# Performance work log

Measured on AMD Instinct MI355X. Metric: run time of the kernel, lower is better.

Reference implementation:

```python
import jax, jax.numpy as jnp
import numpy as np

HEADS = 16
DIM_HEAD = 64
SEG = 512            # total_segment_len (num_longterm_mem_tokens = 0)
THETA = 10000.0
NEG_INF = -1e30


def _rotate_half(t):
    # interleaved pair rotation, as in rotary-embedding-torch
    t2 = t.reshape(*t.shape[:-1], t.shape[-1] // 2, 2)
    return jnp.stack((-t2[..., 1], t2[..., 0]), axis=-1).reshape(t.shape)


def setup_inputs() -> dict:
    key = jax.random.key(0)
    ks = jax.random.split(key, 4)
    b, n, d = 2, 4096, 1024
    dim_inner = HEADS * DIM_HEAD
    seq = jax.random.normal(ks[0], (b, n, d), dtype=jnp.float32)
    g_norm = jnp.ones((d,), dtype=jnp.float32)
    W_qkv = jax.random.normal(ks[1], (d, 3 * dim_inner), dtype=jnp.float32) * (d ** -0.5)
    W_out = jax.random.normal(ks[2], (dim_inner, d), dtype=jnp.float32) * (dim_inner ** -0.5)
    pm = jax.random.normal(ks[3], (2, HEADS, 16, DIM_HEAD), dtype=jnp.float32) * 0.02
    return {"seq": seq, "g_norm": g_norm, "W_qkv": W_qkv, "W_out": W_out, "pm": pm}


def reference(seq, g_norm, W_qkv, W_out, pm):
    b, n_tot, dim = seq.shape
    p = pm.shape[2]
    dh = DIM_HEAD

    # RMSNorm (elementwise affine, eps = dtype eps as in torch default)
    eps = jnp.asarray(jnp.finfo(seq.dtype).eps, seq.dtype)
    x = seq * jax.lax.rsqrt(jnp.mean(seq * seq, axis=-1, keepdims=True) + eps) * g_norm

    qkv = x @ W_qkv                                   # [b, n, 3*h*dh]
    q, k, v = jnp.split(qkv, 3, axis=-1)

    def split_heads(t):
        return t.reshape(b, n_tot, HEADS, dh).transpose(0, 2, 1, 3)  # b h n d

    q, k, v = map(split_heads, (q, k, v))

    # rotary over global positions (applied before segmenting)
    pos = jnp.arange(n_tot, dtype=seq.dtype)
    inv_freq = 1.0 / (THETA ** (jnp.arange(0, dh, 2, dtype=seq.dtype) / dh))
    ang = jnp.repeat(pos[:, None] * inv_freq, 2, axis=-1)            # [n, dh]
    cos, sin = jnp.cos(ang), jnp.sin(ang)
    q = q * cos + _rotate_half(q) * sin
    k = k * cos + _rotate_half(k) * sin

    # fold segments into batch: b h (w n) d -> (b w) h n d
    w = n_tot // SEG
    def seg_fold(t):
        return t.reshape(b, HEADS, w, SEG, dh).transpose(0, 2, 1, 3, 4).reshape(b * w, HEADS, SEG, dh)
    q, k, v = map(seg_fold, (q, k, v))

    # prepend persistent memory kv
    pmk = jnp.broadcast_to(pm[0], (b * w, HEADS, p, dh))
    pmv = jnp.broadcast_to(pm[1], (b * w, HEADS, p, dh))
    k = jnp.concatenate((pmk, k), axis=-2)            # [(bw), h, p+n, d]
    v = jnp.concatenate((pmv, v), axis=-2)

    scores = jnp.einsum('bhid,bhjd->bhij', q, k) * (dh ** -0.5)
    i = jnp.arange(SEG)[:, None]
    j = jnp.arange(SEG + p)[None, :]
    mask = (j < p) | ((j - p) <= i)                   # persistent mem always visible, causal in-segment
    scores = jnp.where(mask, scores, NEG_INF)
    attn = jax.nn.softmax(scores, axis=-1)
    out = jnp.einsum('bhij,bhjd->bhid', attn, v)      # [(bw), h, n, d]

    out = out.transpose(0, 2, 1, 3).reshape(b * w, SEG, HEADS * dh)
    out = out @ W_out
    return out.reshape(b, n_tot, dim)
```

## Files before the change

kernel.cpp:

```cpp
#include <hip/hip_runtime.h>
#include <hip/hip_bf16.h>

typedef __attribute__((ext_vector_type(8))) short short8v;
typedef __attribute__((ext_vector_type(4))) float f32x4;

#define B_ 2
#define NTOK 4096
#define DMODEL 1024
#define HEADS_ 16
#define DH 64
#define SEG_ 512
#define PMEM 16
#define ROWS 8192
#define QKVC 3072

__global__ __launch_bounds__(256) void rmsnorm_bf16(const float* __restrict__ seq,
                                                    const float* __restrict__ g,
                                                    __hip_bfloat16* __restrict__ x) {
    int row = blockIdx.x;
    const float4* in = (const float4*)(seq + (size_t)row * DMODEL);
    int tid = threadIdx.x;
    float4 v = in[tid];
    float ss = v.x*v.x + v.y*v.y + v.z*v.z + v.w*v.w;
    #pragma unroll
    for (int off = 32; off >= 1; off >>= 1) ss += __shfl_xor(ss, off, 64);
    __shared__ float red[4];
    if ((tid & 63) == 0) red[tid >> 6] = ss;
    __syncthreads();
    float tot = red[0] + red[1] + red[2] + red[3];
    float scale = rsqrtf(tot * (1.0f/(float)DMODEL) + 1.1920929e-7f);
    float4 gv = ((const float4*)g)[tid];
    union { ushort4 u; __hip_bfloat16 h[4]; } pk;
    pk.h[0] = __float2bfloat16(v.x*scale*gv.x);
    pk.h[1] = __float2bfloat16(v.y*scale*gv.y);
    pk.h[2] = __float2bfloat16(v.z*scale*gv.z);
    pk.h[3] = __float2bfloat16(v.w*scale*gv.w);
    ((ushort4*)(x + (size_t)row * DMODEL))[tid] = pk.u;
}

__global__ __launch_bounds__(256) void setup_kernel(float* __restrict__ tab,
                                                    const float* __restrict__ pm,
                                                    __hip_bfloat16* __restrict__ pmb,
                                                    const float* __restrict__ wqkv,
                                                    __hip_bfloat16* __restrict__ wqkvt,
                                                    const float* __restrict__ wout,
                                                    __hip_bfloat16* __restrict__ woutt) {
    __shared__ float t[32][33];
    int b = blockIdx.x;
    if (b < 640) {
        int idx = b*256 + threadIdx.x;
        if (idx < NTOK*32) {
            int n = idx >> 5, p = idx & 31;
            float inv = powf(10000.f, -(float)p * (1.f/32.f));
            float a = (float)n * inv;
            float sn, cs;
            sincosf(a, &sn, &cs);
            float* tp = tab + (size_t)n*64;
            tp[2*p]     = cs;
            tp[2*p + 1] = sn;
        } else {
            int j = idx - NTOK*32;
            pmb[j] = __float2bfloat16(pm[j]);
        }
        return;
    }
    b -= 640;
    const float* W; __hip_bfloat16* Wt; int N, n0, k0;
    if (b < 3072) { W = wqkv; Wt = wqkvt; N = QKVC;   n0 = (b % 96)*32; k0 = (b / 96)*32; }
    else { b -= 3072; W = wout; Wt = woutt; N = DMODEL; n0 = (b % 32)*32; k0 = (b / 32)*32; }
    int c = threadIdx.x & 31, r = threadIdx.x >> 5;
    #pragma unroll
    for (int rr = 0; rr < 32; rr += 8)
        t[rr + r][c] = W[(size_t)(k0 + rr + r)*N + n0 + c];
    __syncthreads();
    #pragma unroll
    for (int rr = 0; rr < 32; rr += 8)
        Wt[(size_t)(n0 + rr + r)*DMODEL + k0 + c] = __float2bfloat16(t[c][rr + r]);
}

__device__ __forceinline__ void gldl(const __hip_bfloat16* g, char* l) {
    __builtin_amdgcn_global_load_lds((const __attribute__((address_space(1))) void*)g,
                                     (__attribute__((address_space(3))) void*)l, 16, 0, 0);
}
__device__ __forceinline__ void storeC(float* p, float v) { *p = v; }
__device__ __forceinline__ void storeC(__hip_bfloat16* p, float v) { *p = __float2bfloat16(v); }

template<typename OutT, bool ROPE>
__global__ __launch_bounds__(256, 2) void gemm_t(const __hip_bfloat16* __restrict__ A,
                                                 const __hip_bfloat16* __restrict__ Bt,
                                                 OutT* __restrict__ C,
                                                 const float* __restrict__ tab,
                                                 int M, int N, int K) {
    __shared__ __align__(16) char smem[32768];
    const int tid = threadIdx.x;
    const int wid = tid >> 6, lane = tid & 63;
    const int q8 = gridDim.x >> 3;
    const int swz = (blockIdx.x & 7) * q8 + (blockIdx.x >> 3);
    const int nbx = N >> 7;
    const int bm = (swz / nbx) * 128, bn = (swz % nbx) * 128;
    const int wm = (wid >> 1) * 64, wn = (wid & 1) * 64;
    const int fr = lane & 15, g = lane >> 4;

    const int srow = tid >> 3;
    const int scol = ((tid & 7) ^ (srow & 7)) * 8;
    const __hip_bfloat16* Asrc = A  + (size_t)(bm + srow)*K + scol;
    const __hip_bfloat16* Bsrc = Bt + (size_t)(bn + srow)*K + scol;

    f32x4 acc[4][4];
    #pragma unroll
    for (int i = 0; i < 4; ++i)
        #pragma unroll
        for (int j = 0; j < 4; ++j)
            acc[i][j] = (f32x4){0.f, 0.f, 0.f, 0.f};

    for (int k0 = 0; k0 < K; k0 += 64) {
        #pragma unroll
        for (int i = 0; i < 4; ++i)
            gldl(Asrc + (size_t)i*32*K + k0, smem + i*4096 + tid*16);
        #pragma unroll
        for (int i = 0; i < 4; ++i)
            gldl(Bsrc + (size_t)i*32*K + k0, smem + 16384 + i*4096 + tid*16);
        __syncthreads();

        short8v a[4][2], b[4][2];
        #pragma unroll
        for (int mt = 0; mt < 4; ++mt) {
            int row = wm + mt*16 + fr;
            #pragma unroll
            for (int ks = 0; ks < 2; ++ks)
                a[mt][ks] = *(const short8v*)(smem + row*128 + ((ks*64 + g*16) ^ ((fr&7)<<4)));
        }
        #pragma unroll
        for (int nt = 0; nt < 4; ++nt) {
            int row = wn + nt*16 + fr;
            #pragma unroll
            for (int ks = 0; ks < 2; ++ks)
                b[nt][ks] = *(const short8v*)(smem + 16384 + row*128 + ((ks*64 + g*16) ^ ((fr&7)<<4)));
        }
        #pragma unroll
        for (int mt = 0; mt < 4; ++mt)
            #pragma unroll
            for (int nt = 0; nt < 4; ++nt)
                #pragma unroll
                for (int ks = 0; ks < 2; ++ks)
                    acc[mt][nt] = __builtin_amdgcn_mfma_f32_16x16x32_bf16(a[mt][ks], b[nt][ks], acc[mt][nt], 0, 0, 0);
        __syncthreads();
    }

    const int rsub = (lane >> 4) << 2;
    if (ROPE && bn < 2048) {
        #pragma unroll
        for (int mt = 0; mt < 4; ++mt) {
            int rbase = bm + wm + mt*16 + rsub;
            #pragma unroll
            for (int nt = 0; nt < 4; ++nt) {
                int col = bn + wn + nt*16 + fr;
                int d = col & 63;
                int dc = d & ~1;
                #pragma unroll
                for (int r = 0; r < 4; ++r) {
                    float v = acc[mt][nt][r];
                    float pv = __shfl_xor(v, 1, 64);
                    int n = (rbase + r) & (NTOK - 1);
                    const float* tb = tab + (size_t)n*64;
                    float cs = tb[dc], sn = tb[dc+1];
                    float o = v*cs + ((d & 1) ? pv*sn : -pv*sn);
                    storeC(&C[(size_t)(rbase + r)*N + col], (float)o);
                }
            }
        }
    } else {
        #pragma unroll
        for (int mt = 0; mt < 4; ++mt) {
            int rbase = bm + wm + mt*16 + rsub;
            #pragma unroll
            for (int nt = 0; nt < 4; ++nt) {
                int col = bn + wn + nt*16 + fr;
                #pragma unroll
                for (int r = 0; r < 4; ++r)
                    storeC(&C[(size_t)(rbase + r)*N + col], acc[mt][nt][r]);
            }
        }
    }
}

__device__ __forceinline__ void stage_load(const __hip_bfloat16* __restrict__ qkv,
                                           const __hip_bfloat16* __restrict__ pmb,
                                           int h, int srow, int tt, int skey, int sdg,
                                           uint4 kv[2]) {
    int kg = tt*64 + skey;
    if (kg < PMEM) {
        kv[0] = *(const uint4*)(pmb + ((size_t)h*PMEM + kg)*DH + sdg);
        kv[1] = *(const uint4*)(pmb + ((size_t)(HEADS_ + h)*PMEM + kg)*DH + sdg);
    } else {
        int r = min(kg - PMEM, SEG_ - 1);
        const __hip_bfloat16* bp = qkv + (size_t)(srow + r)*QKVC + h*DH + sdg;
        kv[0] = *(const uint4*)(bp + 1024);
        kv[1] = *(const uint4*)(bp + 2048);
    }
}

__device__ __forceinline__ void stage_write(char* Kb, char* Vb,
                                            int skey, int sdg, const uint4 kv[2]) {
    *(uint4*)(Kb + ((skey*128 + sdg*2) ^ ((skey&7)<<4))) = kv[0];
    union { uint4 u; ushort s[8]; } vv; vv.u = kv[1];
    #pragma unroll
    for (int j = 0; j < 8; ++j) {
        int d = sdg + j;
        *(ushort*)(Vb + ((d*128 + skey*2) ^ ((d&7)<<4))) = vv.s[j];
    }
}

__global__ __launch_bounds__(512, 2) void attn_mfma(const __hip_bfloat16* __restrict__ qkv,
                                                    const __hip_bfloat16* __restrict__ pmb,
                                                    __hip_bfloat16* __restrict__ ao) {
    __shared__ __hip_bfloat16 KB[2][4096];
    __shared__ __hip_bfloat16 VB[2][4096];
    __shared__ __hip_bfloat16 PB[8][1024];

    const int bid = blockIdx.x;
    const int xcd = bid & 7, ii = bid >> 3;
    const int s  = 2*xcd + (ii >> 5);
    const int h  = ii & 15;
    const int rb = (ii >> 4) & 1;
    const int srow = (s >> 3)*NTOK + (s & 7)*SEG_;
    const int tid = threadIdx.x;
    const int w = tid >> 6, lane = tid & 63;
    const int g = lane >> 4, fr = lane & 15;
    const int rsub = g * 4;
    char* Pw = (char*)&PB[w][0];

    const int grp0 = 2*w + rb;
    const int grp1 = 30 - 2*w + rb;
    const int tmax = 7 + rb;

    short8v aq[2][2];
    #pragma unroll
    for (int mt = 0; mt < 2; ++mt) {
        int grp = mt ? grp1 : grp0;
        const __hip_bfloat16* qp = qkv + (size_t)(srow + grp*16 + fr)*QKVC + h*DH;
        #pragma unroll
        for (int ks = 0; ks < 2; ++ks)
            aq[mt][ks] = *(const short8v*)(qp + ks*32 + g*8);
    }

    f32x4 accO[2][4];
    float l_[2][4];
    #pragma unroll
    for (int mt = 0; mt < 2; ++mt) {
        #pragma unroll
        for (int dt = 0; dt < 4; ++dt) accO[mt][dt] = (f32x4){0.f,0.f,0.f,0.f};
        #pragma unroll
        for (int r = 0; r < 4; ++r) l_[mt][r] = 0.f;
    }

    const int skey = tid >> 3, sdg = (tid & 7) * 8;

    {
        uint4 kv[2];
        stage_load(qkv, pmb, h, srow, 0, skey, sdg, kv);
        stage_write((char*)&KB[0][0], (char*)&VB[0][0], skey, sdg, kv);
    }
    __syncthreads();

    for (int t = 0; t <= tmax; ++t) {
        const int bf = t & 1;
        uint4 kvn[2];
        if (t < tmax) stage_load(qkv, pmb, h, srow, t + 1, skey, sdg, kvn);

        char* Kb = (char*)&KB[bf][0];
        char* Vb = (char*)&VB[bf][0];

        short8v bk[4][2];
        #pragma unroll
        for (int nt = 0; nt < 4; ++nt)
            #pragma unroll
            for (int ks = 0; ks < 2; ++ks) {
                int row = nt*16 + fr;
                bk[nt][ks] = *(const short8v*)(Kb + ((row*128 + ks*64 + g*16) ^ ((row&7)<<4)));
            }

        #pragma unroll
        for (int mt = 0; mt < 2; ++mt) {
            const int qb = (mt ? grp1 : grp0) * 16;
            if (t > 0 && t*64 > qb + 31) continue;

            f32x4 sA[4];
            #pragma unroll
            for (int nt = 0; nt < 4; ++nt) sA[nt] = (f32x4){0.f,0.f,0.f,0.f};
            __builtin_amdgcn_s_setprio(1);
            #pragma unroll
            for (int ks = 0; ks < 2; ++ks)
                #pragma unroll
                for (int nt = 0; nt < 4; ++nt)
                    sA[nt] = __builtin_amdgcn_mfma_f32_16x16x32_bf16(aq[mt][ks], bk[nt][ks], sA[nt], 0, 0, 0);
            __builtin_amdgcn_s_setprio(0);

            if (!(t*64 + 63 <= qb + 16)) {
                #pragma unroll
                for (int nt = 0; nt < 4; ++nt) {
                    int kg2 = t*64 + nt*16 + fr;
                    #pragma unroll
                    for (int r = 0; r < 4; ++r) {
                        int irow = qb + rsub + r;
                        if (!((kg2 < PMEM) || (kg2 <= irow + PMEM))) sA[nt][r] = -1e30f;
                    }
                }
            }

            #pragma unroll
            for (int nt = 0; nt < 4; ++nt)
                #pragma unroll
                for (int r = 0; r < 4; ++r)
                    sA[nt][r] = __expf(fmaf(sA[nt][r], 0.125f, -8.0f));
            #pragma unroll
            for (int r = 0; r < 4; ++r)
                l_[mt][r] += sA[0][r] + sA[1][r] + sA[2][r] + sA[3][r];

            #pragma unroll
            for (int nt = 0; nt < 4; ++nt)
                #pragma unroll
                for (int r = 0; r < 4; ++r) {
                    int row_l = rsub + r;
                    *(__hip_bfloat16*)(Pw + ((row_l*128 + (nt*16 + fr)*2) ^ ((row_l&7)<<4))) =
                        __float2bfloat16(sA[nt][r]);
                }

            __builtin_amdgcn_s_setprio(1);
            #pragma unroll
            for (int ks2 = 0; ks2 < 2; ++ks2) {
                short8v ap = *(const short8v*)(Pw + ((fr*128 + ks2*64 + g*16) ^ ((fr&7)<<4)));
                #pragma unroll
                for (int dt = 0; dt < 4; ++dt) {
                    int vrow = dt*16 + fr;
                    short8v bv = *(const short8v*)(Vb + ((vrow*128 + ks2*64 + g*16) ^ ((vrow&7)<<4)));
                    accO[mt][dt] = __builtin_amdgcn_mfma_f32_16x16x32_bf16(ap, bv, accO[mt][dt], 0, 0, 0);
                }
            }
            __builtin_amdgcn_s_setprio(0);
        }

        if (t < tmax) stage_write((char*)&KB[bf^1][0], (char*)&VB[bf^1][0], skey, sdg, kvn);
        __syncthreads();
    }

    #pragma unroll
    for (int mt = 0; mt < 2; ++mt) {
        const int grp = mt ? grp1 : grp0;
        float inv[4];
        #pragma unroll
        for (int r = 0; r < 4; ++r) {
            float lt = l_[mt][r];
            #pragma unroll
            for (int off = 1; off <= 8; off <<= 1) lt += __shfl_xor(lt, off, 64);
            inv[r] = 1.0f / lt;
        }
        #pragma unroll
        for (int dt = 0; dt < 4; ++dt)
            #pragma unroll
            for (int r = 0; r < 4; ++r) {
                int row_l = rsub + r;
                *(__hip_bfloat16*)(Pw + ((row_l*128 + (dt*16 + fr)*2) ^ ((row_l&7)<<4))) =
                    __float2bfloat16(accO[mt][dt][r] * inv[r]);
            }
        #pragma unroll
        for (int c = 0; c < 2; ++c) {
            int row_l = c*8 + (lane >> 3);
            size_t grow = (size_t)(srow + grp*16 + row_l);
            uint4 v = *(const uint4*)(Pw + ((row_l*128 + (lane&7)*16) ^ ((row_l&7)<<4)));
            *(uint4*)((char*)(ao + grow*DMODEL + h*DH) + (lane&7)*16) = v;
        }
    }
}

extern "C" void kernel_launch(void* const* d_in, const int* in_sizes, int n_in,
                              void* d_out, int out_size, void* d_ws, size_t ws_size,
                              hipStream_t stream) {
    const float* seq  = (const float*)d_in[0];
    const float* g    = (const float*)d_in[1];
    const float* wqkv = (const float*)d_in[2];
    const float* wout = (const float*)d_in[3];
    const float* pm   = (const float*)d_in[4];
    float* out = (float*)d_out;

    char* ws = (char*)d_ws;
    __hip_bfloat16* qkvb  = (__hip_bfloat16*)ws;
    __hip_bfloat16* xb    = (__hip_bfloat16*)(ws + 50331648);
    __hip_bfloat16* wqkvt = (__hip_bfloat16*)(ws + 50331648 + 16777216);
    __hip_bfloat16* woutt = (__hip_bfloat16*)(ws + 50331648 + 16777216 + 6291456);
    float* tab            = (float*)(ws + 50331648 + 16777216 + 6291456 + 2097152);
    __hip_bfloat16* pmb   = (__hip_bfloat16*)(ws + 50331648 + 16777216 + 6291456 + 2097152 + 1048576);

    setup_kernel<<<4736, 256, 0, stream>>>(tab, pm, pmb, wqkv, wqkvt, wout, woutt);
    rmsnorm_bf16<<<ROWS, 256, 0, stream>>>(seq, g, xb);
    gemm_t<__hip_bfloat16, true><<<(QKVC/128)*(ROWS/128), 256, 0, stream>>>(xb, wqkvt, qkvb, tab, ROWS, QKVC, DMODEL);
    attn_mfma<<<512, 512, 0, stream>>>(qkvb, pmb, xb);
    gemm_t<float, false><<<(DMODEL/128)*(ROWS/128), 256, 0, stream>>>(xb, woutt, out, nullptr, ROWS, DMODEL, DMODEL);
}
```

Measured before the change: 147.1 us.

## Add warp-specialized producer/consumer GEMM for QKV projection with RoPE epilogue

Replaces the QKV projection GEMM with a 512-thread kernel where four producer waves stream A/B tiles from global memory through registers into double-buffered LDS, while four consumer waves run MFMA with raised priority. The intent is to overlap global loads with matrix math instead of relying on the previous global_load_lds path with per-iteration syncs. The cost is 64KB of shared memory per block, which lowers occupancy, plus more barriers per tile. The old ROPE branch is removed from gemm_t since only the output GEMM still uses it.

```diff
diff --git a/kernel.cpp b/kernel.cpp
--- a/kernel.cpp
+++ b/kernel.cpp
@@ -85,6 +85,135 @@
 __device__ __forceinline__ void storeC(float* p, float v) { *p = v; }
 __device__ __forceinline__ void storeC(__hip_bfloat16* p, float v) { *p = __float2bfloat16(v); }
 
+__global__ __launch_bounds__(512, 2) void gemm_pc(const __hip_bfloat16* __restrict__ A,
+                                                  const __hip_bfloat16* __restrict__ Bt,
+                                                  __hip_bfloat16* __restrict__ C,
+                                                  const float* __restrict__ tab) {
+    __shared__ __align__(16) char smem[65536];
+    const int tid = threadIdx.x;
+    const int wid = tid >> 6, lane = tid & 63;
+    const int q8 = gridDim.x >> 3;
+    const int swz = (blockIdx.x & 7) * q8 + (blockIdx.x >> 3);
+    const int nbx = QKVC >> 7;
+    const int bm = (swz / nbx) * 128, bn = (swz % nbx) * 128;
+    const int K = DMODEL;
+
+    if (wid >= 4) {
+        const int ptid = tid - 256;
+        const int srow = ptid >> 3;
+        const int scol = ((ptid & 7) ^ (srow & 7)) * 8;
+        const __hip_bfloat16* Asrc = A  + (size_t)(bm + srow)*K + scol;
+        const __hip_bfloat16* Bsrc = Bt + (size_t)(bn + srow)*K + scol;
+        uint4 ra[4], rb[4];
+        #pragma unroll
+        for (int i = 0; i < 4; ++i) {
+            ra[i] = *(const uint4*)(Asrc + (size_t)i*32*K);
+            rb[i] = *(const uint4*)(Bsrc + (size_t)i*32*K);
+        }
+        #pragma unroll
+        for (int i = 0; i < 4; ++i) {
+            *(uint4*)(smem + i*4096 + ptid*16) = ra[i];
+            *(uint4*)(smem + 16384 + i*4096 + ptid*16) = rb[i];
+        }
+        #pragma unroll
+        for (int i = 0; i < 4; ++i) {
+            ra[i] = *(const uint4*)(Asrc + (size_t)i*32*K + 64);
+            rb[i] = *(const uint4*)(Bsrc + (size_t)i*32*K + 64);
+        }
+        asm volatile("s_waitcnt lgkmcnt(0)" ::: "memory");
+        __builtin_amdgcn_s_barrier();
+        #pragma unroll 1
+        for (int t = 0; t < 16; ++t) {
+            if (t < 15) {
+                char* dst = smem + ((t + 1) & 1)*32768;
+                #pragma unroll
+                for (int i = 0; i < 4; ++i) {
+                    *(uint4*)(dst + i*4096 + ptid*16) = ra[i];
+                    *(uint4*)(dst + 16384 + i*4096 + ptid*16) = rb[i];
+                }
+                if (t < 14) {
+                    const int k0 = (t + 2)*64;
+                    #pragma unroll
+                    for (int i = 0; i < 4; ++i) {
+                        ra[i] = *(const uint4*)(Asrc + (size_t)i*32*K + k0);
+                        rb[i] = *(const uint4*)(Bsrc + (size_t)i*32*K + k0);
+                    }
+                }
+            }
+            asm volatile("s_waitcnt lgkmcnt(0)" ::: "memory");
+            __builtin_amdgcn_s_barrier();
+        }
+        return;
+    }
+
+    const int wm = (wid >> 1) * 64, wn = (wid & 1) * 64;
+    const int fr = lane & 15, g = lane >> 4;
+
+    f32x4 acc[4][4];
+    #pragma unroll
+    for (int i = 0; i < 4; ++i)
+        #pragma unroll
+        for (int j = 0; j < 4; ++j)
+            acc[i][j] = (f32x4){0.f, 0.f, 0.f, 0.f};
+
+    __builtin_amdgcn_s_barrier();
+    #pragma unroll 1
+    for (int t = 0; t < 16; ++t) {
+        const char* buf = smem + (t & 1)*32768;
+        short8v a[4][2], b[4][2];
+        #pragma unroll
+        for (int mt = 0; mt < 4; ++mt) {
+            int row = wm + mt*16 + fr;
+            #pragma unroll
+            for (int ks = 0; ks < 2; ++ks)
+                a[mt][ks] = *(const short8v*)(buf + row*128 + ((ks*64 + g*16) ^ ((fr&7)<<4)));
+        }
+        #pragma unroll
+        for (int nt = 0; nt < 4; ++nt) {
+            int row = wn + nt*16 + fr;
+            #pragma unroll
+            for (int ks = 0; ks < 2; ++ks)
+                b[nt][ks] = *(const short8v*)(buf + 16384 + row*128 + ((ks*64 + g*16) ^ ((fr&7)<<4)));
+        }
+        __builtin_amdgcn_s_setprio(1);
+        #pragma unroll
+        for (int mt = 0; mt < 4; ++mt)
+            #pragma unroll
+            for (int nt = 0; nt < 4; ++nt)
+                #pragma unroll
+                for (int ks = 0; ks < 2; ++ks)
+                    acc[mt][nt] = __builtin_amdgcn_mfma_f32_16x16x32_bf16(a[mt][ks], b[nt][ks], acc[mt][nt], 0, 0, 0);
+        __builtin_amdgcn_s_setprio(0);
+        __builtin_amdgcn_s_barrier();
+    }
+
+    const int rsub = (lane >> 4) << 2;
+    const bool dorope = (bn < 2048);
+    #pragma unroll
+    for (int mt = 0; mt < 4; ++mt) {
+        int rbase = bm + wm + mt*16 + rsub;
+        #pragma unroll
+        for (int nt = 0; nt < 4; ++nt) {
+            int col = bn + wn + nt*16 + fr;
+            int d = col & 63;
+            int dc = d & ~1;
+            #pragma unroll
+            for (int r = 0; r < 4; ++r) {
+                float v = acc[mt][nt][r];
+                float pv = __shfl_xor(v, 1, 64);
+                float o = v;
+                if (dorope) {
+                    int n = (rbase + r) & (NTOK - 1);
+                    const float* tb = tab + (size_t)n*64;
+                    float cs = tb[dc], sn = tb[dc+1];
+                    o = v*cs + ((d & 1) ? pv*sn : -pv*sn);
+                }
+                storeC(&C[(size_t)(rbase + r)*QKVC + col], o);
+            }
+        }
+    }
+}
+
 template<typename OutT, bool ROPE>
 __global__ __launch_bounds__(256, 2) void gemm_t(const __hip_bfloat16* __restrict__ A,
                                                  const __hip_bfloat16* __restrict__ Bt,
@@ -148,38 +277,15 @@
     }
 
     const int rsub = (lane >> 4) << 2;
-    if (ROPE && bn < 2048) {
-        #pragma unroll
-        for (int mt = 0; mt < 4; ++mt) {
-            int rbase = bm + wm + mt*16 + rsub;
-            #pragma unroll
-            for (int nt = 0; nt < 4; ++nt) {
-                int col = bn + wn + nt*16 + fr;
-                int d = col & 63;
-                int dc = d & ~1;
-                #pragma unroll
-                for (int r = 0; r < 4; ++r) {
-                    float v = acc[mt][nt][r];
-                    float pv = __shfl_xor(v, 1, 64);
-                    int n = (rbase + r) & (NTOK - 1);
-                    const float* tb = tab + (size_t)n*64;
-                    float cs = tb[dc], sn = tb[dc+1];
-                    float o = v*cs + ((d & 1) ? pv*sn : -pv*sn);
-                    storeC(&C[(size_t)(rbase + r)*N + col], (float)o);
-                }
-            }
-        }
-    } else {
-        #pragma unroll
-        for (int mt = 0; mt < 4; ++mt) {
-            int rbase = bm + wm + mt*16 + rsub;
-            #pragma unroll
-            for (int nt = 0; nt < 4; ++nt) {
-                int col = bn + wn + nt*16 + fr;
-                #pragma unroll
-                for (int r = 0; r < 4; ++r)
-                    storeC(&C[(size_t)(rbase + r)*N + col], acc[mt][nt][r]);
-            }
+    #pragma unroll
+    for (int mt = 0; mt < 4; ++mt) {
+        int rbase = bm + wm + mt*16 + rsub;
+        #pragma unroll
+        for (int nt = 0; nt < 4; ++nt) {
+            int col = bn + wn + nt*16 + fr;
+            #pragma unroll
+            for (int r = 0; r < 4; ++r)
+                storeC(&C[(size_t)(rbase + r)*N + col], acc[mt][nt][r]);
         }
     }
 }
@@ -393,7 +499,7 @@
 
     setup_kernel<<<4736, 256, 0, stream>>>(tab, pm, pmb, wqkv, wqkvt, wout, woutt);
     rmsnorm_bf16<<<ROWS, 256, 0, stream>>>(seq, g, xb);
-    gemm_t<__hip_bfloat16, true><<<(QKVC/128)*(ROWS/128), 256, 0, stream>>>(xb, wqkvt, qkvb, tab, ROWS, QKVC, DMODEL);
+    gemm_pc<<<(QKVC/128)*(ROWS/128), 512, 0, stream>>>(xb, wqkvt, qkvb, tab);
     attn_mfma<<<512, 512, 0, stream>>>(qkvb, pmb, xb);
     gemm_t<float, false><<<(DMODEL/128)*(ROWS/128), 256, 0, stream>>>(xb, woutt, out, nullptr, ROWS, DMODEL, DMODEL);
 }
```

Measured after the change: 299.4 us. 2.04x slower.
